# Optimization experiments

Hardware: AMD Instinct MI355X
Metric: run time of the kernel (lower is better)

Reference implementation:

```python
import jax, jax.numpy as jnp
import numpy as np


def conv1x1(x, W, b):
    # x: [B,C,H,W], W: [O,C], b: [O]  (torch Conv2d 1x1 squeezed)
    return jnp.einsum('oc,bchw->bohw', W, x) + b[None, :, None, None]


def setup_inputs() -> dict:
    key = jax.random.key(0)
    ks = jax.random.split(key, 7)
    B, C, H, W = 8, 256, 32, 32
    s = 1.0 / np.sqrt(C)
    x = jax.random.normal(ks[0], (B, C, H, W), jnp.float32)
    Wq = jax.random.normal(ks[1], (C, C), jnp.float32) * s
    bq = jax.random.normal(ks[2], (C,), jnp.float32) * 0.01
    Wk = jax.random.normal(ks[3], (C, C), jnp.float32) * s
    bk = jax.random.normal(ks[4], (C,), jnp.float32) * 0.01
    Wo = jax.random.normal(ks[5], (C, C), jnp.float32) * s
    bo = jax.random.normal(ks[6], (C,), jnp.float32) * 0.01
    return {"x": x, "Wq": Wq, "bq": bq, "Wk": Wk, "bk": bk, "Wo": Wo, "bo": bo}


def reference(x, Wq, bq, Wk, bk, Wo, bo):
    B, C, H, W = x.shape
    HW = H * W
    scale = 1.0 / (C ** 0.5)
    # proj_query: torch does view(B,C,HW).permute(0,2,1).transpose(1,2).contiguous().view(-1,C)
    # which is a row-major reshape of [B,C,HW] into [B*HW, C] (channel/spatial interleaved).
    # Reproduced faithfully.
    q = conv1x1(x, Wq, bq).reshape(B, C, HW).reshape(-1, C)          # [B*HW, C]
    # proj_key: view(B,C,HW).transpose(0,1).contiguous().view(C,-1) -> true [C, B*HW]
    k = jnp.transpose(conv1x1(x, Wk, bk).reshape(B, C, HW), (1, 0, 2)).reshape(C, -1)
    x_w = (q @ k).reshape(B * HW, B, HW)                              # [BHW, B, HW]
    out_co = jnp.max(x_w, axis=-1) + jnp.mean(x_w, axis=-1)           # [BHW, B]
    x_co = jnp.mean(out_co, axis=-1).reshape(B, HW) * scale           # [B, HW]
    x_co = jax.nn.softmax(x_co, axis=-1).reshape(B, 1, H, W)
    return conv1x1(x * x_co, Wo, bo)
```

## Files before the change

### kernel.cpp

```cpp
#include <hip/hip_runtime.h>

#define BATCH 8
#define CH 256
#define HWSZ 1024
#define BHW 8192

typedef _Float16 f16;
typedef _Float16 f16x4 __attribute__((ext_vector_type(4)));
typedef _Float16 f16x8 __attribute__((ext_vector_type(8)));
typedef float f32x4 __attribute__((ext_vector_type(4)));
typedef unsigned long long u64;
typedef __attribute__((address_space(3))) unsigned int lds_u32;
typedef __attribute__((address_space(1))) const unsigned int glob_u32;

__global__ __launch_bounds__(256) void xmean_kernel(const float* __restrict__ x,
                                                    float* __restrict__ xmean)
{
    const int row  = blockIdx.x * 8 + (threadIdx.x >> 5);
    const int part = threadIdx.x & 31;
    const float4* p = (const float4*)(x + (size_t)row * HWSZ);
    float s = 0.f;
#pragma unroll
    for (int i = 0; i < 8; ++i) { float4 v = p[i * 32 + part]; s += v.x + v.y + v.z + v.w; }
    s += __shfl_xor(s, 1, 64);
    s += __shfl_xor(s, 2, 64);
    s += __shfl_xor(s, 4, 64);
    s += __shfl_xor(s, 8, 64);
    s += __shfl_xor(s, 16, 64);
    if (part == 0) xmean[row] = s * (1.0f / HWSZ);
}

__global__ __launch_bounds__(256) void kmeanW_kernel(
    const float* __restrict__ Wk, const float* __restrict__ bk,
    const float* __restrict__ xmean, float* __restrict__ kmean)
{
    __shared__ float xm[CH];
    const int b = blockIdx.x;
    const int tid = threadIdx.x;
    xm[tid] = xmean[b * 256 + tid];
    __syncthreads();

    float acc = 0.f;
    const float4* w = (const float4*)(Wk + tid * CH);
    for (int c4 = 0; c4 < 64; ++c4) {
        float4 wv = w[c4];
        acc = fmaf(wv.x, xm[c4 * 4 + 0], acc);
        acc = fmaf(wv.y, xm[c4 * 4 + 1], acc);
        acc = fmaf(wv.z, xm[c4 * 4 + 2], acc);
        acc = fmaf(wv.w, xm[c4 * 4 + 3], acc);
    }
    kmean[b * 256 + tid] = acc + bk[tid];
}

__global__ __launch_bounds__(512, 1) void pgemmQK_kernel(
    const float* __restrict__ x,
    const float* __restrict__ Wq, const float* __restrict__ Wk,
    const float* __restrict__ bq, const float* __restrict__ bk,
    f16* __restrict__ Qh, char* __restrict__ Ksw)
{
    __shared__ __align__(16) char kbuf[32 * 1024];
    __shared__ __align__(16) float xt[256][36];
    f16* tile = (f16*)&xt[0][0];
    char* tileb = (char*)&xt[0][0];

    const int pxg0 = blockIdx.x * 32;
    const int b    = pxg0 >> 10;
    const int hw0  = pxg0 & 1023;
    const int tid  = threadIdx.x;
    const int lane = tid & 63;
    const int wid  = tid >> 6;
    const int m = lane & 15, g = lane >> 4;

    {
        const int f4 = tid & 7;
        const int cs = tid >> 3;
#pragma unroll
        for (int pass = 0; pass < 4; ++pass) {
            const int c = pass * 64 + cs;
            float4 v = *(const float4*)(x + ((size_t)b * CH + c) * HWSZ + hw0 + f4 * 4);
            *(float4*)&xt[c][f4 * 4] = v;
        }
    }
    __syncthreads();

    {
        const int px = tid & 31;
        const int q8 = tid >> 5;
        const int sw = (px & 7) << 4;
#pragma unroll
        for (int r = 0; r < 2; ++r) {
            f16x8 hi, lo;
#pragma unroll
            for (int i = 0; i < 8; ++i) {
                const int c = q8 * 16 + r * 8 + i;
                float v = xt[c][px];
                f16 h = (f16)v;
                hi[i] = h;
                lo[i] = (f16)(v - (float)h);
            }
            const int base = q8 * 32 + r * 16;
            *(f16x8*)(kbuf + px * 1024 + (base ^ sw)) = hi;
            *(f16x8*)(kbuf + px * 1024 + 512 + (base ^ sw)) = lo;
        }
    }

    f16x8 a[2][8];
#define LOAD_W(Wsel)                                                                     \
    {                                                                                    \
        _Pragma("unroll")                                                                \
        for (int t = 0; t < 2; ++t)                                                      \
            _Pragma("unroll")                                                            \
            for (int kk = 0; kk < 8; ++kk) {                                             \
                const float* wrow = (Wsel) + (size_t)(wid * 32 + t * 16 + m) * CH + kk * 32 + g * 8; \
                float4 w0 = *(const float4*)(wrow);                                      \
                float4 w1 = *(const float4*)(wrow + 4);                                  \
                f16x8 av;                                                                \
                av[0] = (f16)w0.x; av[1] = (f16)w0.y; av[2] = (f16)w0.z; av[3] = (f16)w0.w; \
                av[4] = (f16)w1.x; av[5] = (f16)w1.y; av[6] = (f16)w1.z; av[7] = (f16)w1.w; \
                a[t][kk] = av;                                                           \
            }                                                                            \
    }
    LOAD_W(Wq);
    __syncthreads();

    const int sw0 = (m & 7) << 4;
    const f32x4 vz = {0.f, 0.f, 0.f, 0.f};
    f32x4 acc[2][2];

#define MFMA_PASS()                                                                      \
    {                                                                                    \
        _Pragma("unroll")                                                                \
        for (int t = 0; t < 2; ++t) { acc[t][0] = vz; acc[t][1] = vz; }                  \
        _Pragma("unroll")                                                                \
        for (int ks = 0; ks < 16; ++ks) {                                                \
            const int X = ks * 64 + g * 16;                                              \
            f16x8 b0 = *(const f16x8*)(kbuf + m * 1024 + (X ^ sw0));                     \
            f16x8 b1 = *(const f16x8*)(kbuf + (16 + m) * 1024 + (X ^ sw0));              \
            _Pragma("unroll")                                                            \
            for (int t = 0; t < 2; ++t) {                                                \
                acc[t][0] = __builtin_amdgcn_mfma_f32_16x16x32_f16(a[t][ks & 7], b0, acc[t][0], 0, 0, 0); \
                acc[t][1] = __builtin_amdgcn_mfma_f32_16x16x32_f16(a[t][ks & 7], b1, acc[t][1], 0, 0, 0); \
            }                                                                            \
        }                                                                                \
    }

    MFMA_PASS();

#pragma unroll
    for (int t = 0; t < 2; ++t) {
        const int co0 = wid * 32 + t * 16 + 4 * g;
        float4 bv = *(const float4*)(bq + co0);
        float ba[4] = {bv.x, bv.y, bv.z, bv.w};
#pragma unroll
        for (int u = 0; u < 2; ++u) {
            const int px = u * 16 + m;
#pragma unroll
            for (int j = 0; j < 4; ++j)
                tile[(co0 + j) * 32 + (px ^ (j << 3))] = (f16)(acc[t][u][j] + ba[j]);
        }
    }
    __syncthreads();
#pragma unroll
    for (int pass = 0; pass < 2; ++pass) {
        const int co  = pass * 128 + (tid >> 2);
        const int run = tid & 3;
        f16x8 v = *(const f16x8*)(tile + co * 32 + ((run * 8) ^ ((co & 3) << 3)));
        *(f16x8*)(Qh + ((size_t)b * CH + co) * HWSZ + hw0 + run * 8) = v;
    }

    LOAD_W(Wk);
    MFMA_PASS();
    __syncthreads();

#pragma unroll
    for (int t = 0; t < 2; ++t) {
        const int co0 = wid * 32 + t * 16 + 4 * g;
        float4 bv = *(const float4*)(bk + co0);
        float ba[4] = {bv.x, bv.y, bv.z, bv.w};
#pragma unroll
        for (int u = 0; u < 2; ++u) {
            const int px = u * 16 + m;
            f16x4 pk;
#pragma unroll
            for (int j = 0; j < 4; ++j) pk[j] = (f16)(acc[t][u][j] + ba[j]);
            *(f16x4*)(tileb + px * 512 + ((co0 * 2) ^ (m << 3))) = pk;
        }
    }
    __syncthreads();
    {
        const int px = tid & 31;
        const int rp = tid >> 5;
        const int kloc = (px & 15) << 3;
        const int kglb = (px & 7) << 4;
        char* grow = Ksw + (size_t)(pxg0 + px) * 512;
#pragma unroll
        for (int i = 0; i < 2; ++i) {
            const int r = rp + i * 16;
            u64 a0 = *(const u64*)(tileb + px * 512 + ((r * 16) ^ kloc));
            u64 a1 = *(const u64*)(tileb + px * 512 + ((r * 16 + 8) ^ kloc));
            char* gdst = grow + ((r * 16) ^ kglb);
            *(u64*)gdst = a0;
            *(u64*)(gdst + 8) = a1;
        }
    }
#undef MFMA_PASS
#undef LOAD_W
}

__global__ __launch_bounds__(256, 2) void score_kernel(
    const f16* __restrict__ Qh, const char* __restrict__ Ksw, float* __restrict__ rowmax)
{
    __shared__ __align__(16) char kbuf[2][32768];
    __shared__ float lds_rm[128][2];

    const int batch = blockIdx.x & 7;
    const int r0    = (blockIdx.x >> 3) * 128;
    const int tid   = threadIdx.x;
    const int lane  = tid & 63;
    const int wid   = tid >> 6;
    const int wr = wid >> 1, wc = wid & 1;
    const int m = lane & 15, g = lane >> 4;
    const int rbase = r0 + wr * 64;

    const char* kbase = Ksw + (size_t)batch * HWSZ * 512;

#define STAGE(buf, ch)                                                                   \
    {                                                                                    \
        const char* _src = kbase + (ch) * 64 * 512 + tid * 16;                           \
        char* _dst = &kbuf[buf][tid * 16];                                               \
        _Pragma("unroll")                                                                \
        for (int k = 0; k < 8; ++k)                                                      \
            __builtin_amdgcn_global_load_lds((glob_u32*)(_src + k * 4096),               \
                                             (lds_u32*)(_dst + k * 4096), 16, 0, 0);     \
    }

    STAGE(0, 0);

    f16x8 a[4][8];
#pragma unroll
    for (int t = 0; t < 4; ++t)
#pragma unroll
        for (int kk = 0; kk < 8; ++kk)
            a[t][kk] = *(const f16x8*)(Qh + (size_t)(rbase + t * 16 + m) * CH + kk * 32 + 8 * g);

    int boff[8][2];
    {
        const int sw = (m & 7) << 4;
#pragma unroll
        for (int kk = 0; kk < 8; ++kk)
#pragma unroll
            for (int u2 = 0; u2 < 2; ++u2) {
                const int col = wc * 32 + u2 * 16 + m;
                boff[kk][u2] = col * 512 + ((kk * 64 + g * 16) ^ sw);
            }
    }

    float rm[4][4];
#pragma unroll
    for (int t = 0; t < 4; ++t)
#pragma unroll
        for (int jj = 0; jj < 4; ++jj) rm[t][jj] = -1e30f;

    int cur = 0;
    for (int ch = 0; ch < 16; ++ch) {
        if (ch < 15) {
            STAGE(cur ^ 1, ch + 1);
            asm volatile("s_waitcnt vmcnt(8)" ::: "memory");
        } else {
            asm volatile("s_waitcnt vmcnt(0)" ::: "memory");
        }
        __builtin_amdgcn_s_barrier();

        const char* kb = &kbuf[cur][0];
        f32x4 acc[4][2];
        const f32x4 vz = {0.f, 0.f, 0.f, 0.f};
#pragma unroll
        for (int t = 0; t < 4; ++t) { acc[t][0] = vz; acc[t][1] = vz; }

#pragma unroll
        for (int kk = 0; kk < 8; ++kk) {
            f16x8 bfr[2];
            bfr[0] = *(const f16x8*)(kb + boff[kk][0]);
            bfr[1] = *(const f16x8*)(kb + boff[kk][1]);
#pragma unroll
            for (int t = 0; t < 4; ++t) {
                acc[t][0] = __builtin_amdgcn_mfma_f32_16x16x32_f16(a[t][kk], bfr[0], acc[t][0], 0, 0, 0);
                acc[t][1] = __builtin_amdgcn_mfma_f32_16x16x32_f16(a[t][kk], bfr[1], acc[t][1], 0, 0, 0);
            }
        }

#pragma unroll
        for (int t = 0; t < 4; ++t)
#pragma unroll
            for (int jj = 0; jj < 4; ++jj)
                rm[t][jj] = fmaxf(rm[t][jj], fmaxf(acc[t][0][jj], acc[t][1][jj]));

        asm volatile("" ::: "memory");
        __builtin_amdgcn_s_barrier();
        cur ^= 1;
    }
#undef STAGE

#pragma unroll
    for (int d = 1; d < 16; d <<= 1)
#pragma unroll
        for (int t = 0; t < 4; ++t)
#pragma unroll
            for (int jj = 0; jj < 4; ++jj)
                rm[t][jj] = fmaxf(rm[t][jj], __shfl_xor(rm[t][jj], d, 64));

    if (m == 0) {
#pragma unroll
        for (int t = 0; t < 4; ++t)
#pragma unroll
            for (int jj = 0; jj < 4; ++jj)
                lds_rm[wr * 64 + t * 16 + g * 4 + jj][wc] = rm[t][jj];
    }
    __syncthreads();
    if (tid < 128)
        rowmax[(size_t)(r0 + tid) * BATCH + batch] = fmaxf(lds_rm[tid][0], lds_rm[tid][1]);
}

__global__ __launch_bounds__(256) void logits_kernel(
    const f16* __restrict__ Qh, const float* __restrict__ kmean,
    const float* __restrict__ rowmax, float* __restrict__ logits)
{
    __shared__ float km[BATCH][CH];
    const int tid = threadIdx.x;
#pragma unroll
    for (int i = 0; i < 8; ++i) km[i][tid] = kmean[i * 256 + tid];
    __syncthreads();

    const int r = blockIdx.x * 256 + tid;
    float acc[8];
#pragma unroll
    for (int b = 0; b < 8; ++b) acc[b] = 0.f;

    const f16x8* q = (const f16x8*)(Qh + (size_t)r * CH);
    for (int c8 = 0; c8 < 32; ++c8) {
        f16x8 qv = q[c8];
        float qf[8];
#pragma unroll
        for (int i = 0; i < 8; ++i) qf[i] = (float)qv[i];
#pragma unroll
        for (int b = 0; b < 8; ++b) {
            float4 k0 = *(const float4*)&km[b][c8 * 8];
            float4 k1 = *(const float4*)&km[b][c8 * 8 + 4];
            acc[b] = fmaf(qf[0], k0.x, acc[b]); acc[b] = fmaf(qf[1], k0.y, acc[b]);
            acc[b] = fmaf(qf[2], k0.z, acc[b]); acc[b] = fmaf(qf[3], k0.w, acc[b]);
            acc[b] = fmaf(qf[4], k1.x, acc[b]); acc[b] = fmaf(qf[5], k1.y, acc[b]);
            acc[b] = fmaf(qf[6], k1.z, acc[b]); acc[b] = fmaf(qf[7], k1.w, acc[b]);
        }
    }
    float lg = 0.f;
#pragma unroll
    for (int b = 0; b < 8; ++b) lg += rowmax[(size_t)r * 8 + b] + acc[b];
    logits[r] = lg * (1.0f / 128.0f);
}

__global__ __launch_bounds__(256) void softmax_kernel(const float* __restrict__ logits,
                                                      float* __restrict__ wgt)
{
    const int br = blockIdx.x, tid = threadIdx.x;
    __shared__ float red[256];
    float l[4];
#pragma unroll
    for (int i = 0; i < 4; ++i) l[i] = logits[br * HWSZ + i * 256 + tid];

    float mx = fmaxf(fmaxf(l[0], l[1]), fmaxf(l[2], l[3]));
    red[tid] = mx;
    __syncthreads();
    for (int s = 128; s > 0; s >>= 1) {
        if (tid < s) red[tid] = fmaxf(red[tid], red[tid + s]);
        __syncthreads();
    }
    mx = red[0];
    __syncthreads();

    float e[4], sm = 0.f;
#pragma unroll
    for (int i = 0; i < 4; ++i) { e[i] = expf(l[i] - mx); sm += e[i]; }
    red[tid] = sm;
    __syncthreads();
    for (int s = 128; s > 0; s >>= 1) {
        if (tid < s) red[tid] += red[tid + s];
        __syncthreads();
    }
    const float inv = 1.0f / red[0];
#pragma unroll
    for (int i = 0; i < 4; ++i)
        wgt[br * HWSZ + i * 256 + tid] = e[i] * inv;
}

__global__ __launch_bounds__(512, 1) void pgemmY_kernel(
    const float* __restrict__ x, const float* __restrict__ Wo, const float* __restrict__ bo,
    const float* __restrict__ wgt, float* __restrict__ out)
{
    __shared__ __align__(16) char kbuf[16 * 1024];
    __shared__ __align__(16) float xt[256][36];

    const int pxg0 = blockIdx.x * 32;
    const int b    = pxg0 >> 10;
    const int hw0  = pxg0 & 1023;
    const int tid  = threadIdx.x;
    const int lane = tid & 63;
    const int wid  = tid >> 6;
    const int m = lane & 15, g = lane >> 4;

    {
        const int f4 = tid & 7;
        const int cs = tid >> 3;
#pragma unroll
        for (int pass = 0; pass < 4; ++pass) {
            const int c = pass * 64 + cs;
            float4 v = *(const float4*)(x + ((size_t)b * CH + c) * HWSZ + hw0 + f4 * 4);
            *(float4*)&xt[c][f4 * 4] = v;
        }
    }
    __syncthreads();

    {
        const int px = tid & 31;
        const int q8 = tid >> 5;
        const int sw = (px & 7) << 4;
#pragma unroll
        for (int r = 0; r < 2; ++r) {
            f16x8 hi;
#pragma unroll
            for (int i = 0; i < 8; ++i)
                hi[i] = (f16)xt[q8 * 16 + r * 8 + i][px];
            *(f16x8*)(kbuf + px * 512 + ((q8 * 32 + r * 16) ^ sw)) = hi;
        }
    }

    f16x8 a[2][8];
#pragma unroll
    for (int t = 0; t < 2; ++t)
#pragma unroll
        for (int kk = 0; kk < 8; ++kk) {
            const float* wrow = Wo + (size_t)(wid * 32 + t * 16 + m) * CH + kk * 32 + g * 8;
            float4 w0 = *(const float4*)(wrow);
            float4 w1 = *(const float4*)(wrow + 4);
            f16x8 av;
            av[0] = (f16)w0.x; av[1] = (f16)w0.y; av[2] = (f16)w0.z; av[3] = (f16)w0.w;
            av[4] = (f16)w1.x; av[5] = (f16)w1.y; av[6] = (f16)w1.z; av[7] = (f16)w1.w;
            a[t][kk] = av;
        }

    __syncthreads();

    f32x4 acc[2][2];
    const f32x4 vz = {0.f, 0.f, 0.f, 0.f};
#pragma unroll
    for (int t = 0; t < 2; ++t) { acc[t][0] = vz; acc[t][1] = vz; }

    const int sw0 = (m & 7) << 4;
#pragma unroll
    for (int ks = 0; ks < 8; ++ks) {
        const int X = ks * 64 + g * 16;
        f16x8 b0 = *(const f16x8*)(kbuf + m * 512 + (X ^ sw0));
        f16x8 b1 = *(const f16x8*)(kbuf + (16 + m) * 512 + (X ^ sw0));
#pragma unroll
        for (int t = 0; t < 2; ++t) {
            acc[t][0] = __builtin_amdgcn_mfma_f32_16x16x32_f16(a[t][ks], b0, acc[t][0], 0, 0, 0);
            acc[t][1] = __builtin_amdgcn_mfma_f32_16x16x32_f16(a[t][ks], b1, acc[t][1], 0, 0, 0);
        }
    }

    float wv[2];
    wv[0] = wgt[b * HWSZ + hw0 + m];
    wv[1] = wgt[b * HWSZ + hw0 + 16 + m];
#pragma unroll
    for (int t = 0; t < 2; ++t) {
        const int co0 = wid * 32 + t * 16 + 4 * g;
        float4 bv = *(const float4*)(bo + co0);
        float ba[4] = {bv.x, bv.y, bv.z, bv.w};
#pragma unroll
        for (int u = 0; u < 2; ++u)
#pragma unroll
            for (int j = 0; j < 4; ++j)
                out[((size_t)b * CH + co0 + j) * HWSZ + hw0 + u * 16 + m] =
                    fmaf(acc[t][u][j], wv[u], ba[j]);
    }
}

extern "C" void kernel_launch(void* const* d_in, const int* in_sizes, int n_in,
                              void* d_out, int out_size, void* d_ws, size_t ws_size,
                              hipStream_t stream)
{
    const float* x  = (const float*)d_in[0];
    const float* Wq = (const float*)d_in[1];
    const float* bq = (const float*)d_in[2];
    const float* Wk = (const float*)d_in[3];
    const float* bk = (const float*)d_in[4];
    const float* Wo = (const float*)d_in[5];
    const float* bo = (const float*)d_in[6];
    float* out = (float*)d_out;

    char* ws = (char*)d_ws;
    f16*   Qh     = (f16*)(ws);
    char*  Ksw    = (char*)(ws + (4 << 20));
    float* rowmax = (float*)(ws + (8 << 20));
    float* kmean  = (float*)(ws + (8 << 20) + (256 << 10));
    float* xmean  = (float*)(ws + (8 << 20) + (264 << 10));
    float* logits = (float*)(ws + (8 << 20) + (272 << 10));
    float* wgt    = (float*)(ws + (8 << 20) + (304 << 10));

    xmean_kernel  <<<dim3(256),  256, 0, stream>>>(x, xmean);
    kmeanW_kernel <<<dim3(8),    256, 0, stream>>>(Wk, bk, xmean, kmean);
    pgemmQK_kernel<<<dim3(256),  512, 0, stream>>>(x, Wq, Wk, bq, bk, Qh, Ksw);
    score_kernel  <<<dim3(512),  256, 0, stream>>>(Qh, Ksw, rowmax);
    logits_kernel <<<dim3(32),   256, 0, stream>>>(Qh, kmean, rowmax, logits);
    softmax_kernel<<<dim3(8),    256, 0, stream>>>(logits, wgt);
    pgemmY_kernel <<<dim3(256),  512, 0, stream>>>(x, Wo, bo, wgt, out);
}
```

Measured before the change: 102.5 us.

## Fuse Wo projection into QK GEMM, merge logits into score, drop xmean pass

Computes the output projection Wo·x alongside Q and K in a single pass over x, stores it as fp16, and applies the softmax gate and bias in a lightweight elementwise kernel. It moves the x-mean reduction into the same kernel with atomics and folds the Q·kmean logits term into the score kernel, which accumulates into logits with atomics. The aim is fewer kernel launches and fewer reads of x. In exchange it writes and reads an extra fp16 intermediate, adds a memset, relies on float atomics whose order is not deterministic, and lowers precision by rounding Y to fp16 before gating.

```diff
diff --git a/kernel.cpp b/kernel.cpp
--- a/kernel.cpp
+++ b/kernel.cpp
@@ -13,31 +13,14 @@
 typedef __attribute__((address_space(3))) unsigned int lds_u32;
 typedef __attribute__((address_space(1))) const unsigned int glob_u32;
 
-__global__ __launch_bounds__(256) void xmean_kernel(const float* __restrict__ x,
-                                                    float* __restrict__ xmean)
-{
-    const int row  = blockIdx.x * 8 + (threadIdx.x >> 5);
-    const int part = threadIdx.x & 31;
-    const float4* p = (const float4*)(x + (size_t)row * HWSZ);
-    float s = 0.f;
-#pragma unroll
-    for (int i = 0; i < 8; ++i) { float4 v = p[i * 32 + part]; s += v.x + v.y + v.z + v.w; }
-    s += __shfl_xor(s, 1, 64);
-    s += __shfl_xor(s, 2, 64);
-    s += __shfl_xor(s, 4, 64);
-    s += __shfl_xor(s, 8, 64);
-    s += __shfl_xor(s, 16, 64);
-    if (part == 0) xmean[row] = s * (1.0f / HWSZ);
-}
-
 __global__ __launch_bounds__(256) void kmeanW_kernel(
     const float* __restrict__ Wk, const float* __restrict__ bk,
-    const float* __restrict__ xmean, float* __restrict__ kmean)
+    const float* __restrict__ xsum, float* __restrict__ kmean)
 {
     __shared__ float xm[CH];
     const int b = blockIdx.x;
     const int tid = threadIdx.x;
-    xm[tid] = xmean[b * 256 + tid];
+    xm[tid] = xsum[b * 256 + tid] * (1.0f / HWSZ);
     __syncthreads();
 
     float acc = 0.f;
@@ -52,11 +35,12 @@
     kmean[b * 256 + tid] = acc + bk[tid];
 }
 
-__global__ __launch_bounds__(512, 1) void pgemmQK_kernel(
+__global__ __launch_bounds__(512, 1) void pgemmQKY_kernel(
     const float* __restrict__ x,
-    const float* __restrict__ Wq, const float* __restrict__ Wk,
+    const float* __restrict__ Wq, const float* __restrict__ Wk, const float* __restrict__ Wo,
     const float* __restrict__ bq, const float* __restrict__ bk,
-    f16* __restrict__ Qh, char* __restrict__ Ksw)
+    f16* __restrict__ Qh, char* __restrict__ Ksw, f16* __restrict__ Yh,
+    float* __restrict__ xsum)
 {
     __shared__ __align__(16) char kbuf[32 * 1024];
     __shared__ __align__(16) float xt[256][36];
@@ -104,8 +88,18 @@
         }
     }
 
-    f16x8 a[2][8];
-#define LOAD_W(Wsel)                                                                     \
+    if (tid < 256) {
+        float s = 0.f;
+#pragma unroll
+        for (int i4 = 0; i4 < 8; ++i4) {
+            float4 v = *(const float4*)&xt[tid][i4 * 4];
+            s += v.x + v.y + v.z + v.w;
+        }
+        atomicAdd(&xsum[b * 256 + tid], s);
+    }
+
+    f16x8 aA[2][8], aB[2][8];
+#define LOAD_W(dst, Wsel)                                                                \
     {                                                                                    \
         _Pragma("unroll")                                                                \
         for (int t = 0; t < 2; ++t)                                                      \
@@ -117,34 +111,35 @@
                 f16x8 av;                                                                \
                 av[0] = (f16)w0.x; av[1] = (f16)w0.y; av[2] = (f16)w0.z; av[3] = (f16)w0.w; \
                 av[4] = (f16)w1.x; av[5] = (f16)w1.y; av[6] = (f16)w1.z; av[7] = (f16)w1.w; \
-                a[t][kk] = av;                                                           \
+                dst[t][kk] = av;                                                         \
             }                                                                            \
     }
-    LOAD_W(Wq);
+    LOAD_W(aA, Wq);
     __syncthreads();
 
     const int sw0 = (m & 7) << 4;
     const f32x4 vz = {0.f, 0.f, 0.f, 0.f};
     f32x4 acc[2][2];
 
-#define MFMA_PASS()                                                                      \
+#define MFMA_PASS(ARR, NKS)                                                              \
     {                                                                                    \
         _Pragma("unroll")                                                                \
         for (int t = 0; t < 2; ++t) { acc[t][0] = vz; acc[t][1] = vz; }                  \
         _Pragma("unroll")                                                                \
-        for (int ks = 0; ks < 16; ++ks) {                                                \
+        for (int ks = 0; ks < (NKS); ++ks) {                                             \
             const int X = ks * 64 + g * 16;                                              \
             f16x8 b0 = *(const f16x8*)(kbuf + m * 1024 + (X ^ sw0));                     \
             f16x8 b1 = *(const f16x8*)(kbuf + (16 + m) * 1024 + (X ^ sw0));              \
             _Pragma("unroll")                                                            \
             for (int t = 0; t < 2; ++t) {                                                \
-                acc[t][0] = __builtin_amdgcn_mfma_f32_16x16x32_f16(a[t][ks & 7], b0, acc[t][0], 0, 0, 0); \
-                acc[t][1] = __builtin_amdgcn_mfma_f32_16x16x32_f16(a[t][ks & 7], b1, acc[t][1], 0, 0, 0); \
+                acc[t][0] = __builtin_amdgcn_mfma_f32_16x16x32_f16(ARR[t][ks & 7], b0, acc[t][0], 0, 0, 0); \
+                acc[t][1] = __builtin_amdgcn_mfma_f32_16x16x32_f16(ARR[t][ks & 7], b1, acc[t][1], 0, 0, 0); \
             }                                                                            \
         }                                                                                \
     }
 
-    MFMA_PASS();
+    MFMA_PASS(aA, 16);
+    LOAD_W(aB, Wk);
 
 #pragma unroll
     for (int t = 0; t < 2; ++t) {
@@ -168,8 +163,8 @@
         *(f16x8*)(Qh + ((size_t)b * CH + co) * HWSZ + hw0 + run * 8) = v;
     }
 
-    LOAD_W(Wk);
-    MFMA_PASS();
+    MFMA_PASS(aB, 16);
+    LOAD_W(aA, Wo);
     __syncthreads();
 
 #pragma unroll
@@ -203,15 +198,41 @@
             *(u64*)(gdst + 8) = a1;
         }
     }
+
+    MFMA_PASS(aA, 8);
+    __syncthreads();
+
+#pragma unroll
+    for (int t = 0; t < 2; ++t) {
+        const int co0 = wid * 32 + t * 16 + 4 * g;
+#pragma unroll
+        for (int u = 0; u < 2; ++u) {
+            const int px = u * 16 + m;
+#pragma unroll
+            for (int j = 0; j < 4; ++j)
+                tile[(co0 + j) * 32 + (px ^ (j << 3))] = (f16)acc[t][u][j];
+        }
+    }
+    __syncthreads();
+#pragma unroll
+    for (int pass = 0; pass < 2; ++pass) {
+        const int co  = pass * 128 + (tid >> 2);
+        const int run = tid & 3;
+        f16x8 v = *(const f16x8*)(tile + co * 32 + ((run * 8) ^ ((co & 3) << 3)));
+        *(f16x8*)(Yh + ((size_t)b * CH + co) * HWSZ + hw0 + run * 8) = v;
+    }
 #undef MFMA_PASS
 #undef LOAD_W
 }
 
 __global__ __launch_bounds__(256, 2) void score_kernel(
-    const f16* __restrict__ Qh, const char* __restrict__ Ksw, float* __restrict__ rowmax)
+    const f16* __restrict__ Qh, const char* __restrict__ Ksw,
+    const float* __restrict__ kmean, float* __restrict__ logits)
 {
     __shared__ __align__(16) char kbuf[2][32768];
     __shared__ float lds_rm[128][2];
+    __shared__ float lds_dq[128];
+    __shared__ float km[CH];
 
     const int batch = blockIdx.x & 7;
     const int r0    = (blockIdx.x >> 3) * 128;
@@ -222,6 +243,8 @@
     const int m = lane & 15, g = lane >> 4;
     const int rbase = r0 + wr * 64;
 
+    km[tid] = kmean[batch * 256 + tid];
+
     const char* kbase = Ksw + (size_t)batch * HWSZ * 512;
 
 #define STAGE(buf, ch)                                                                   \
@@ -309,6 +332,20 @@
             for (int jj = 0; jj < 4; ++jj)
                 rm[t][jj] = fmaxf(rm[t][jj], __shfl_xor(rm[t][jj], d, 64));
 
+    float dq[4];
+#pragma unroll
+    for (int t = 0; t < 4; ++t) {
+        float s = 0.f;
+#pragma unroll
+        for (int kk = 0; kk < 8; ++kk)
+#pragma unroll
+            for (int i = 0; i < 8; ++i)
+                s = fmaf((float)a[t][kk][i], km[kk * 32 + 8 * g + i], s);
+        s += __shfl_xor(s, 16, 64);
+        s += __shfl_xor(s, 32, 64);
+        dq[t] = s;
+    }
+
     if (m == 0) {
 #pragma unroll
         for (int t = 0; t < 4; ++t)
@@ -316,46 +353,16 @@
             for (int jj = 0; jj < 4; ++jj)
                 lds_rm[wr * 64 + t * 16 + g * 4 + jj][wc] = rm[t][jj];
     }
-    __syncthreads();
-    if (tid < 128)
-        rowmax[(size_t)(r0 + tid) * BATCH + batch] = fmaxf(lds_rm[tid][0], lds_rm[tid][1]);
-}
-
-__global__ __launch_bounds__(256) void logits_kernel(
-    const f16* __restrict__ Qh, const float* __restrict__ kmean,
-    const float* __restrict__ rowmax, float* __restrict__ logits)
-{
-    __shared__ float km[BATCH][CH];
-    const int tid = threadIdx.x;
-#pragma unroll
-    for (int i = 0; i < 8; ++i) km[i][tid] = kmean[i * 256 + tid];
-    __syncthreads();
-
-    const int r = blockIdx.x * 256 + tid;
-    float acc[8];
-#pragma unroll
-    for (int b = 0; b < 8; ++b) acc[b] = 0.f;
-
-    const f16x8* q = (const f16x8*)(Qh + (size_t)r * CH);
-    for (int c8 = 0; c8 < 32; ++c8) {
-        f16x8 qv = q[c8];
-        float qf[8];
-#pragma unroll
-        for (int i = 0; i < 8; ++i) qf[i] = (float)qv[i];
-#pragma unroll
-        for (int b = 0; b < 8; ++b) {
-            float4 k0 = *(const float4*)&km[b][c8 * 8];
-            float4 k1 = *(const float4*)&km[b][c8 * 8 + 4];
-            acc[b] = fmaf(qf[0], k0.x, acc[b]); acc[b] = fmaf(qf[1], k0.y, acc[b]);
-            acc[b] = fmaf(qf[2], k0.z, acc[b]); acc[b] = fmaf(qf[3], k0.w, acc[b]);
-            acc[b] = fmaf(qf[4], k1.x, acc[b]); acc[b] = fmaf(qf[5], k1.y, acc[b]);
-            acc[b] = fmaf(qf[6], k1.z, acc[b]); acc[b] = fmaf(qf[7], k1.w, acc[b]);
-        }
-    }
-    float lg = 0.f;
-#pragma unroll
-    for (int b = 0; b < 8; ++b) lg += rowmax[(size_t)r * 8 + b] + acc[b];
-    logits[r] = lg * (1.0f / 128.0f);
+    if (wc == 0 && lane < 16) {
+#pragma unroll
+        for (int t = 0; t < 4; ++t)
+            lds_dq[wr * 64 + t * 16 + lane] = dq[t];
+    }
+    __syncthreads();
+    if (tid < 128) {
+        float v = fmaxf(lds_rm[tid][0], lds_rm[tid][1]) + lds_dq[tid];
+        atomicAdd(logits + r0 + tid, v * (1.0f / 128.0f));
+    }
 }
 
 __global__ __launch_bounds__(256) void softmax_kernel(const float* __restrict__ logits,
@@ -392,96 +399,28 @@
         wgt[br * HWSZ + i * 256 + tid] = e[i] * inv;
 }
 
-__global__ __launch_bounds__(512, 1) void pgemmY_kernel(
-    const float* __restrict__ x, const float* __restrict__ Wo, const float* __restrict__ bo,
-    const float* __restrict__ wgt, float* __restrict__ out)
-{
-    __shared__ __align__(16) char kbuf[16 * 1024];
-    __shared__ __align__(16) float xt[256][36];
-
-    const int pxg0 = blockIdx.x * 32;
-    const int b    = pxg0 >> 10;
-    const int hw0  = pxg0 & 1023;
-    const int tid  = threadIdx.x;
-    const int lane = tid & 63;
-    const int wid  = tid >> 6;
-    const int m = lane & 15, g = lane >> 4;
-
-    {
-        const int f4 = tid & 7;
-        const int cs = tid >> 3;
-#pragma unroll
-        for (int pass = 0; pass < 4; ++pass) {
-            const int c = pass * 64 + cs;
-            float4 v = *(const float4*)(x + ((size_t)b * CH + c) * HWSZ + hw0 + f4 * 4);
-            *(float4*)&xt[c][f4 * 4] = v;
-        }
-    }
-    __syncthreads();
-
-    {
-        const int px = tid & 31;
-        const int q8 = tid >> 5;
-        const int sw = (px & 7) << 4;
-#pragma unroll
-        for (int r = 0; r < 2; ++r) {
-            f16x8 hi;
-#pragma unroll
-            for (int i = 0; i < 8; ++i)
-                hi[i] = (f16)xt[q8 * 16 + r * 8 + i][px];
-            *(f16x8*)(kbuf + px * 512 + ((q8 * 32 + r * 16) ^ sw)) = hi;
-        }
-    }
-
-    f16x8 a[2][8];
-#pragma unroll
-    for (int t = 0; t < 2; ++t)
-#pragma unroll
-        for (int kk = 0; kk < 8; ++kk) {
-            const float* wrow = Wo + (size_t)(wid * 32 + t * 16 + m) * CH + kk * 32 + g * 8;
-            float4 w0 = *(const float4*)(wrow);
-            float4 w1 = *(const float4*)(wrow + 4);
-            f16x8 av;
-            av[0] = (f16)w0.x; av[1] = (f16)w0.y; av[2] = (f16)w0.z; av[3] = (f16)w0.w;
-            av[4] = (f16)w1.x; av[5] = (f16)w1.y; av[6] = (f16)w1.z; av[7] = (f16)w1.w;
-            a[t][kk] = av;
-        }
-
-    __syncthreads();
-
-    f32x4 acc[2][2];
-    const f32x4 vz = {0.f, 0.f, 0.f, 0.f};
-#pragma unroll
-    for (int t = 0; t < 2; ++t) { acc[t][0] = vz; acc[t][1] = vz; }
-
-    const int sw0 = (m & 7) << 4;
-#pragma unroll
-    for (int ks = 0; ks < 8; ++ks) {
-        const int X = ks * 64 + g * 16;
-        f16x8 b0 = *(const f16x8*)(kbuf + m * 512 + (X ^ sw0));
-        f16x8 b1 = *(const f16x8*)(kbuf + (16 + m) * 512 + (X ^ sw0));
-#pragma unroll
-        for (int t = 0; t < 2; ++t) {
-            acc[t][0] = __builtin_amdgcn_mfma_f32_16x16x32_f16(a[t][ks], b0, acc[t][0], 0, 0, 0);
-            acc[t][1] = __builtin_amdgcn_mfma_f32_16x16x32_f16(a[t][ks], b1, acc[t][1], 0, 0, 0);
-        }
-    }
-
-    float wv[2];
-    wv[0] = wgt[b * HWSZ + hw0 + m];
-    wv[1] = wgt[b * HWSZ + hw0 + 16 + m];
-#pragma unroll
-    for (int t = 0; t < 2; ++t) {
-        const int co0 = wid * 32 + t * 16 + 4 * g;
-        float4 bv = *(const float4*)(bo + co0);
-        float ba[4] = {bv.x, bv.y, bv.z, bv.w};
-#pragma unroll
-        for (int u = 0; u < 2; ++u)
-#pragma unroll
-            for (int j = 0; j < 4; ++j)
-                out[((size_t)b * CH + co0 + j) * HWSZ + hw0 + u * 16 + m] =
-                    fmaf(acc[t][u][j], wv[u], ba[j]);
-    }
+__global__ __launch_bounds__(256) void gateY_kernel(const f16* __restrict__ Yh,
+                                                    const float* __restrict__ wgt,
+                                                    const float* __restrict__ bo,
+                                                    float* __restrict__ out)
+{
+    const size_t idx = ((size_t)blockIdx.x * 256 + threadIdx.x) * 8;
+    const int b  = (int)(idx >> 18);
+    const int c  = (int)(idx >> 10) & 255;
+    const int hw = (int)idx & 1023;
+
+    f16x8 y = *(const f16x8*)(Yh + idx);
+    float4 w0 = *(const float4*)(wgt + b * HWSZ + hw);
+    float4 w1 = *(const float4*)(wgt + b * HWSZ + hw + 4);
+    const float bov = bo[c];
+
+    float4 o0, o1;
+    o0.x = fmaf((float)y[0], w0.x, bov); o0.y = fmaf((float)y[1], w0.y, bov);
+    o0.z = fmaf((float)y[2], w0.z, bov); o0.w = fmaf((float)y[3], w0.w, bov);
+    o1.x = fmaf((float)y[4], w1.x, bov); o1.y = fmaf((float)y[5], w1.y, bov);
+    o1.z = fmaf((float)y[6], w1.z, bov); o1.w = fmaf((float)y[7], w1.w, bov);
+    *(float4*)(out + idx)     = o0;
+    *(float4*)(out + idx + 4) = o1;
 }
 
 extern "C" void kernel_launch(void* const* d_in, const int* in_sizes, int n_in,
@@ -500,17 +439,17 @@
     char* ws = (char*)d_ws;
     f16*   Qh     = (f16*)(ws);
     char*  Ksw    = (char*)(ws + (4 << 20));
-    float* rowmax = (float*)(ws + (8 << 20));
-    float* kmean  = (float*)(ws + (8 << 20) + (256 << 10));
-    float* xmean  = (float*)(ws + (8 << 20) + (264 << 10));
-    float* logits = (float*)(ws + (8 << 20) + (272 << 10));
-    float* wgt    = (float*)(ws + (8 << 20) + (304 << 10));
-
-    xmean_kernel  <<<dim3(256),  256, 0, stream>>>(x, xmean);
-    kmeanW_kernel <<<dim3(8),    256, 0, stream>>>(Wk, bk, xmean, kmean);
-    pgemmQK_kernel<<<dim3(256),  512, 0, stream>>>(x, Wq, Wk, bq, bk, Qh, Ksw);
-    score_kernel  <<<dim3(512),  256, 0, stream>>>(Qh, Ksw, rowmax);
-    logits_kernel <<<dim3(32),   256, 0, stream>>>(Qh, kmean, rowmax, logits);
-    softmax_kernel<<<dim3(8),    256, 0, stream>>>(logits, wgt);
-    pgemmY_kernel <<<dim3(256),  512, 0, stream>>>(x, Wo, bo, wgt, out);
-}
+    f16*   Yh     = (f16*)(ws + (8 << 20));
+    float* xsum   = (float*)(ws + (12 << 20));
+    float* logits = (float*)(ws + (12 << 20) + (8 << 10));
+    float* kmean  = (float*)(ws + (12 << 20) + (40 << 10));
+    float* wgt    = (float*)(ws + (12 << 20) + (48 << 10));
+
+    hipMemsetAsync(xsum, 0, 40 << 10, stream);
+
+    pgemmQKY_kernel<<<dim3(256),  512, 0, stream>>>(x, Wq, Wk, Wo, bq, bk, Qh, Ksw, Yh, xsum);
+    kmeanW_kernel  <<<dim3(8),    256, 0, stream>>>(Wk, bk, xsum, kmean);
+    score_kernel   <<<dim3(512),  256, 0, stream>>>(Qh, Ksw, kmean, logits);
+    softmax_kernel <<<dim3(8),    256, 0, stream>>>(logits, wgt);
+    gateY_kernel   <<<dim3(1024), 256, 0, stream>>>(Yh, wgt, bo, out);
+}
```

Result: faster. 91.34 us (-10.9%).
